# Kernel optimization log

Hardware: AMD Instinct MI355X
Metric: run time of the kernel (lower is better)

## Reference

```python
import jax, jax.numpy as jnp
import numpy as np

B, T = 128, 1024
V, H, L = 65, 512, 3


def setup_inputs() -> dict:
    key = jax.random.key(0)
    ks = jax.random.split(key, 8)
    s_in = 1.0 / np.sqrt(H)
    return {
        "x_seq": jax.random.randint(ks[0], (B, T), 0, V, dtype=jnp.int32),
        "emb": jax.random.normal(ks[1], (V, H), dtype=jnp.float32) * 0.02,
        "w_ih": jax.random.normal(ks[2], (L, 3 * H, H), dtype=jnp.float32) * s_in,
        "w_hh": jax.random.normal(ks[3], (L, 3 * H, H), dtype=jnp.float32) * s_in,
        "b": jax.random.normal(ks[4], (L, 3 * H), dtype=jnp.float32) * s_in,
        "b_n": jax.random.normal(ks[5], (L, H), dtype=jnp.float32) * s_in,
        "w_out": jax.random.normal(ks[6], (V, H), dtype=jnp.float32) * s_in,
        "b_out": jax.random.normal(ks[7], (V,), dtype=jnp.float32) * s_in,
    }


def _gru_cell(x, h, w_ih_l, w_hh_l, b_l, b_n_l):
    # eqx.nn.GRUCell math: igates = W_ih x + b ; hgates = W_hh h
    ig = x @ w_ih_l.T + b_l          # [B, 3H]
    hg = h @ w_hh_l.T                # [B, 3H]
    ir, iz, i_n = jnp.split(ig, 3, axis=-1)
    hr, hz, h_n = jnp.split(hg, 3, axis=-1)
    r = jax.nn.sigmoid(ir + hr)
    z = jax.nn.sigmoid(iz + hz)
    n = jnp.tanh(i_n + r * (h_n + b_n_l))
    return n + z * (h - n)


def reference(x_seq, emb, w_ih, w_hh, b, b_n, w_out, b_out):
    x_emb = emb[x_seq]                       # [B, T, H] embedding lookup
    x_tbh = jnp.swapaxes(x_emb, 0, 1)        # [T, B, H] scan over time
    h0 = jnp.zeros((L, x_seq.shape[0], H), dtype=x_emb.dtype)

    def step(hs, x):
        new_hs = []
        inp = x
        for i in range(L):                   # fixed small layer loop
            h = _gru_cell(inp, hs[i], w_ih[i], w_hh[i], b[i], b_n[i])
            new_hs.append(h)
            inp = h
        y = inp @ w_out.T + b_out            # [B, V]
        return jnp.stack(new_hs), y

    _, y_seq = jax.lax.scan(step, h0, x_tbh)  # y_seq: [T, B, V]
    return jnp.swapaxes(y_seq, 0, 1)          # [B, T, V]
```

## Files before the change

### kernel.cpp

```cpp
#include <hip/hip_runtime.h>

typedef _Float16 f16;
typedef _Float16 f16x8 __attribute__((ext_vector_type(8)));
typedef float f32x4 __attribute__((ext_vector_type(4)));

#define T_STEPS 1024
#define BATCH 128
#define HID 512
#define VOC 65
#define DRING 8
#define NLWG 192
#define NPWG 20
#define FPAD 16

#define OFF_READY 0
#define OFF_HRING 32768
#define HRING_BYTES (3*DRING*BATCH*HID*2)
#define OFF_WPACK (OFF_HRING + HRING_BYTES)
#define WPACK_BYTES (3*32*65536*2)
#define OFF_WOUT (OFF_WPACK + WPACK_BYTES)
#define WOUT_BYTES (5*16*512*2)
#define OFF_EMB (OFF_WOUT + WOUT_BYTES)

#define HHALF 32768

__device__ __forceinline__ float sigmoidf_(float x){ return 1.0f/(1.0f+__expf(-x)); }
__device__ __forceinline__ float tanhf_(float x){ return 1.0f - 2.0f/(__expf(2.0f*x)+1.0f); }

__device__ __forceinline__ f16x8 ld16_sc(const f16* p) {
  f16x8 r;
  asm volatile("global_load_dwordx4 %0, %1, off sc0 sc1" : "=v"(r) : "v"(p) : "memory");
  return r;
}
__device__ __forceinline__ f16x8 ld16_pl(const f16* p) {
  f16x8 r;
  asm volatile("global_load_dwordx4 %0, %1, off" : "=v"(r) : "v"(p) : "memory");
  return r;
}
__device__ __forceinline__ void st16_sc1(f16* p, f16x8 v){
  asm volatile("global_store_dwordx4 %0, %1, off sc1"::"v"(p),"v"(v):"memory"); }

__global__ void convert_kernel(const float* __restrict__ emb, const float* __restrict__ w_ih,
                               const float* __restrict__ w_hh, const float* __restrict__ w_out,
                               char* __restrict__ ws) {
  f16* wpack = (f16*)(ws + OFF_WPACK);
  f16* wout  = (f16*)(ws + OFF_WOUT);
  f16* embh  = (f16*)(ws + OFF_EMB);
  const int NW = 3*32*65536;
  const int TOT = NW + 40960 + VOC*HID;
  for (int e = blockIdx.x*blockDim.x + threadIdx.x; e < TOT; e += gridDim.x*blockDim.x) {
    if (e < NW) {
      int l = e >> 21, rem = e & 0x1FFFFF;
      int g = rem >> 16, idx = rem & 0xFFFF;
      int gt = idx >> 14, kc = (idx >> 9) & 31, lane = (idx >> 3) & 63, jj = idx & 7;
      int n = lane & 15, q = lane >> 4;
      int k = kc*32 + q*8 + jj, d = g*16 + n;
      int row = (gt==0) ? d : (gt==1) ? 512+d : 1024+d;
      float f = (k < 512) ? w_ih[((size_t)(l*1536+row)<<9) + k]
                          : w_hh[((size_t)(l*1536+row)<<9) + (k-512)];
      f16 h;
      if (gt < 3) h = (f16)f;
      else { f16 hi = (f16)f; h = (f16)((f - (float)hi)*2048.0f); }
      wpack[e] = h;
    } else if (e < NW + 40960) {
      int idx = e - NW;
      int vt = idx >> 13, r2 = idx & 8191;
      int kc = r2 >> 9, lane = (r2 >> 3) & 63, jj = r2 & 7;
      int n = lane & 15, q = lane >> 4;
      int v = vt*16 + n, k = kc*32 + q*8 + jj;
      wout[idx] = (v < VOC) ? (f16)w_out[((size_t)v<<9) + k] : (f16)0.0f;
    } else {
      int idx = e - NW - 40960;
      embh[idx] = (f16)emb[idx];
    }
  }
}

#define KEEP4(K0) asm volatile("" : "+v"(afr[K0]), "+v"(afr[K0+1]), "+v"(afr[K0+2]), "+v"(afr[K0+3]))

#define XCHUNK(K0, NW_) \
  asm volatile("s_waitcnt vmcnt(" #NW_ ")" ::: "memory"); \
  KEEP4(K0); \
  _Pragma("unroll") \
  for (int kc = K0; kc < K0+4; ++kc) { \
    f16x8 wnh = *(const f16x8*)(wlds + (((2*32 + kc)*64 + lane) << 3)); \
    f16x8 wnl = *(const f16x8*)(wlds + (((3*32 + kc)*64 + lane) << 3)); \
    ar   = __builtin_amdgcn_mfma_f32_16x16x32_f16(afr[kc], wr[kc], ar,   0, 0, 0); \
    az   = __builtin_amdgcn_mfma_f32_16x16x32_f16(afr[kc], wz[kc], az,   0, 0, 0); \
    anxh = __builtin_amdgcn_mfma_f32_16x16x32_f16(afr[kc], wnh,    anxh, 0, 0, 0); \
    anxl = __builtin_amdgcn_mfma_f32_16x16x32_f16(afr[kc], wnl,    anxl, 0, 0, 0); \
  }

#define HCHUNK(K0, NW_) \
  asm volatile("s_waitcnt vmcnt(" #NW_ ")" ::: "memory"); \
  KEEP4(K0); \
  _Pragma("unroll") \
  for (int kc = K0; kc < K0+4; ++kc) { \
    f16x8 wnh = *(const f16x8*)(wlds + (((2*32 + kc)*64 + lane) << 3)); \
    f16x8 wnl = *(const f16x8*)(wlds + (((3*32 + kc)*64 + lane) << 3)); \
    ar   = __builtin_amdgcn_mfma_f32_16x16x32_f16(afr[kc], wr[kc], ar,   0, 0, 0); \
    az   = __builtin_amdgcn_mfma_f32_16x16x32_f16(afr[kc], wz[kc], az,   0, 0, 0); \
    anhh = __builtin_amdgcn_mfma_f32_16x16x32_f16(afr[kc], wnh,    anhh, 0, 0, 0); \
    anhl = __builtin_amdgcn_mfma_f32_16x16x32_f16(afr[kc], wnl,    anhl, 0, 0, 0); \
  }

__global__ void __launch_bounds__(256) rnn_kernel(const int* __restrict__ xseq,
                           const float* __restrict__ bias, const float* __restrict__ bias_n,
                           const float* __restrict__ b_out, float* __restrict__ out,
                           char* __restrict__ ws) {
  int* F = (int*)(ws + OFF_READY);
  f16* hring = (f16*)(ws + OFF_HRING);
  const int wg = blockIdx.x;
  const int tid = threadIdx.x;
  const int lane = tid & 63, wv = tid >> 6;
  const int quad = lane >> 4, nlane = lane & 15;

  __shared__ __align__(16) f16 wlds[65536];
  __shared__ __align__(16) f16 wolds[8192];
  __shared__ __align__(16) f16 hstage[64*24];

  if (wg < NLWG) {
    const int l = wg / 64, r = wg % 64, g = r >> 1, bh = r & 1;
    {
      const f16x8* src = (const f16x8*)((const f16*)(ws + OFF_WPACK) + ((size_t)(l*32+g) << 16));
      f16x8* dst = (f16x8*)wlds;
      for (int i = tid; i < 8192; i += 256) dst[i] = src[i];
    }
    const int j = g*16 + nlane;
    const float br  = bias[l*1536 + j];
    const float bz  = bias[l*1536 + 512 + j];
    const float bin = bias[l*1536 + 1024 + j];
    const float bn  = bias_n[l*512 + j];
    const int bm = bh*64 + wv*16 + nlane;
    const int tofs = quad*512 + (wv*16 + nlane)*8;

    const int* selfp = F + (l*64 + bh*32 + (lane & 31))*FPAD;
    const int* upp   = (l > 0) ? (F + ((l-1)*64 + bh*32 + (lane & 31))*FPAD) : F;
    const int* bpp = F; int bpact = 0;
    if (wv == 1) {
      if (l < 2) { if (lane < 32) { bpp = F + ((l+1)*64 + bh*32 + lane)*FPAD; bpact = 1; } }
      else       { if (lane < 10) { bpp = F + (192 + bh*10 + lane)*FPAD;      bpact = 1; } }
    }
    __syncthreads();
    f16x8 wr[32], wz[32];
#pragma unroll
    for (int kc = 0; kc < 32; ++kc) {
      wr[kc] = *(const f16x8*)(wlds + (((0*32 + kc)*64 + lane) << 3));
      wz[kc] = *(const f16x8*)(wlds + (((1*32 + kc)*64 + lane) << 3));
    }
    const f16* embh = (const f16*)(ws + OFF_EMB);
    unsigned short hprev[4] = {0, 0, 0, 0};

    for (int t = 0; t < T_STEPS; ++t) {
      if (wv == 0) {
        if (l > 0 && lane >= 32) {
          const int tgt = t + 1;
          int spins = 0;
          while (1) {
            int v = __hip_atomic_load(upp, __ATOMIC_RELAXED, __HIP_MEMORY_SCOPE_AGENT);
            if (__all(v >= tgt)) break;
            if (++spins > (1 << 22)) break;
            __builtin_amdgcn_s_sleep(1);
          }
        }
      } else if (wv == 1) {
        const int tgt = t - (DRING-1);
        int spins = 0;
        while (1) {
          int v = 0x7FFFFFFF;
          if (bpact) v = __hip_atomic_load(bpp, __ATOMIC_RELAXED, __HIP_MEMORY_SCOPE_AGENT);
          if (__all(v >= tgt)) break;
          if (++spins > (1 << 22)) break;
          __builtin_amdgcn_s_sleep(1);
        }
      }
      __syncthreads();

      const int slot_w = t & (DRING-1), slot_r = (t + DRING - 1) & (DRING-1);
      f16x8 afr[32];
      if (l == 0) {
        int idx = xseq[bm*T_STEPS + t];
        const f16* xr = embh + (size_t)idx*HID + quad*8;
#pragma unroll
        for (int kc = 0; kc < 16; ++kc) afr[kc] = ld16_pl(xr + kc*32);
      } else {
        const f16* xr = hring + (size_t)(((l-1)*DRING + slot_w)*2 + bh)*HHALF + tofs;
#pragma unroll
        for (int kc = 0; kc < 16; ++kc) afr[kc] = ld16_sc(xr + kc*2048);
      }
      if (wv == 0 && lane < 32) {
        int spins = 0;
        while (1) {
          int v = __hip_atomic_load(selfp, __ATOMIC_RELAXED, __HIP_MEMORY_SCOPE_AGENT);
          if (__all(v >= t)) break;
          if (++spins > (1 << 22)) break;
          __builtin_amdgcn_s_sleep(1);
        }
      }
      __syncthreads();
      {
        const f16* hrk = hring + (size_t)((l*DRING + slot_r)*2 + bh)*HHALF + tofs;
#pragma unroll
        for (int kc = 0; kc < 16; ++kc) afr[16 + kc] = ld16_sc(hrk + kc*2048);
      }

      f32x4 ar{0,0,0,0}, az{0,0,0,0}, anxh{0,0,0,0}, anxl{0,0,0,0}, anhh{0,0,0,0}, anhl{0,0,0,0};
      XCHUNK(0, 28)  XCHUNK(4, 24)  XCHUNK(8, 20)   XCHUNK(12, 16)
      HCHUNK(16, 12) HCHUNK(20, 8)  HCHUNK(24, 4)   HCHUNK(28, 0)

#pragma unroll
      for (int i = 0; i < 4; ++i) {
        float rr = sigmoidf_(ar[i] + br);
        float zz = sigmoidf_(az[i] + bz);
        float hn = anhh[i] + anhl[i]*(1.0f/2048.0f) + bn;
        float nn = tanhf_(anxh[i] + anxl[i]*(1.0f/2048.0f) + bin + rr*hn);
        union { unsigned short u; f16 h; } cr; cr.u = hprev[i];
        float hv = nn + zz*((float)cr.h - nn);
        union { f16 h; unsigned short u; } cw; cw.h = (f16)hv;
        hprev[i] = cw.u;
        hstage[(wv*16 + quad*4 + i)*24 + nlane] = cw.h;
      }
      __syncthreads();
      if (tid < 128) {
        int d8i = tid >> 6, row = tid & 63;
        f16x8 v8 = *(const f16x8*)(hstage + row*24 + d8i*8);
        f16* hw = hring + (size_t)((l*DRING + slot_w)*2 + bh)*HHALF
                        + (size_t)(2*g + d8i)*512 + row*8;
        st16_sc1(hw, v8);
      }
      asm volatile("s_waitcnt vmcnt(0)" ::: "memory");
      __syncthreads();
      if (tid == 0)
        __hip_atomic_store(F + (l*64 + bh*32 + g)*FPAD, t + 1,
                           __ATOMIC_RELAXED, __HIP_MEMORY_SCOPE_AGENT);
    }
  } else if (wg < NLWG + NPWG) {
    const int p = wg - NLWG, bt = p / 5, vt = p % 5, half = bt >> 1;
    {
      const f16x8* src = (const f16x8*)((const f16*)(ws + OFF_WOUT) + vt*8192);
      f16x8* dst = (f16x8*)wolds;
      for (int i = tid; i < 1024; i += 256) dst[i] = src[i];
    }
    const int v = vt*16 + nlane;
    const float bo = (v < VOC) ? b_out[v] : 0.0f;
    __syncthreads();
    for (int t = 0; t < T_STEPS; ++t) {
      if (wv == 0) {
        const int tgt = t + 1;
        int spins = 0;
        while (1) {
          int vv = 0x7FFFFFFF;
          if (lane < 32) vv = __hip_atomic_load(F + (2*64 + half*32 + lane)*FPAD,
                                                __ATOMIC_RELAXED, __HIP_MEMORY_SCOPE_AGENT);
          if (__all(vv >= tgt)) break;
          if (++spins > (1 << 22)) break;
          __builtin_amdgcn_s_sleep(1);
        }
      }
      __syncthreads();
      if (wv < 2) {
        const int row_abs = bt*32 + wv*16 + nlane;
        const int bh2 = row_abs >> 6, rih = row_abs & 63;
        const f16* hrow = hring + (size_t)((2*DRING + (t & (DRING-1)))*2 + bh2)*HHALF
                                + quad*512 + rih*8;
        f16x8 af[16];
#pragma unroll
        for (int kc = 0; kc < 16; ++kc) af[kc] = ld16_sc(hrow + kc*2048);
        asm volatile("s_waitcnt vmcnt(0)" ::: "memory");
#pragma unroll
        for (int kc = 0; kc < 16; ++kc) asm volatile("" : "+v"(af[kc]));
        f32x4 acc{0,0,0,0};
#pragma unroll
        for (int kc = 0; kc < 16; ++kc) {
          f16x8 w = *(const f16x8*)(wolds + ((kc*64 + lane) << 3));
          acc = __builtin_amdgcn_mfma_f32_16x16x32_f16(af[kc], w, acc, 0, 0, 0);
        }
        if (v < VOC) {
          const int bmb = bt*32 + wv*16;
#pragma unroll
          for (int i = 0; i < 4; ++i) {
            int bidx = bmb + quad*4 + i;
            out[((size_t)bidx*T_STEPS + t)*VOC + v] = acc[i] + bo;
          }
        }
      }
      __syncthreads();
      if (tid == 0)
        __hip_atomic_store(F + (192 + p)*FPAD, t + 1, __ATOMIC_RELAXED, __HIP_MEMORY_SCOPE_AGENT);
    }
  }
}

extern "C" void kernel_launch(void* const* d_in, const int* in_sizes, int n_in,
                              void* d_out, int out_size, void* d_ws, size_t ws_size,
                              hipStream_t stream) {
  const int*   xseq  = (const int*)d_in[0];
  const float* emb   = (const float*)d_in[1];
  const float* w_ih  = (const float*)d_in[2];
  const float* w_hh  = (const float*)d_in[3];
  const float* b     = (const float*)d_in[4];
  const float* b_n   = (const float*)d_in[5];
  const float* w_out = (const float*)d_in[6];
  const float* b_out = (const float*)d_in[7];
  char* ws = (char*)d_ws;

  (void)hipMemsetAsync(d_ws, 0, OFF_HRING + HRING_BYTES, stream);
  hipLaunchKernelGGL(convert_kernel, dim3(4096), dim3(256), 0, stream,
                     emb, w_ih, w_hh, w_out, ws);
  hipLaunchKernelGGL(rnn_kernel, dim3(NLWG + NPWG), dim3(256), 0, stream,
                     xseq, b, b_n, b_out, (float*)d_out, ws);
}
```

Baseline: 6.919 ms.

## Map each layer/batch-half group onto one XCD and use acquire/release with plain loads

```diff
diff --git a/kernel.cpp b/kernel.cpp
--- a/kernel.cpp
+++ b/kernel.cpp
@@ -9,8 +9,6 @@
 #define HID 512
 #define VOC 65
 #define DRING 8
-#define NLWG 192
-#define NPWG 20
 #define FPAD 16
 
 #define OFF_READY 0
@@ -27,11 +25,6 @@
 __device__ __forceinline__ float sigmoidf_(float x){ return 1.0f/(1.0f+__expf(-x)); }
 __device__ __forceinline__ float tanhf_(float x){ return 1.0f - 2.0f/(__expf(2.0f*x)+1.0f); }
 
-__device__ __forceinline__ f16x8 ld16_sc(const f16* p) {
-  f16x8 r;
-  asm volatile("global_load_dwordx4 %0, %1, off sc0 sc1" : "=v"(r) : "v"(p) : "memory");
-  return r;
-}
 __device__ __forceinline__ f16x8 ld16_pl(const f16* p) {
   f16x8 r;
   asm volatile("global_load_dwordx4 %0, %1, off" : "=v"(r) : "v"(p) : "memory");
@@ -114,13 +107,14 @@
   const int tid = threadIdx.x;
   const int lane = tid & 63, wv = tid >> 6;
   const int quad = lane >> 4, nlane = lane & 15;
+  const int xcd = wg & 7, mem = wg >> 3;
 
   __shared__ __align__(16) f16 wlds[65536];
   __shared__ __align__(16) f16 wolds[8192];
   __shared__ __align__(16) f16 hstage[64*24];
 
-  if (wg < NLWG) {
-    const int l = wg / 64, r = wg % 64, g = r >> 1, bh = r & 1;
+  if (xcd < 6) {
+    const int gid = xcd, l = gid >> 1, bh = gid & 1, g = mem;
     {
       const f16x8* src = (const f16x8*)((const f16*)(ws + OFF_WPACK) + ((size_t)(l*32+g) << 16));
       f16x8* dst = (f16x8*)wlds;
@@ -135,7 +129,9 @@
     const int tofs = quad*512 + (wv*16 + nlane)*8;
 
     const int* selfp = F + (l*64 + bh*32 + (lane & 31))*FPAD;
+    const int* self0 = F + (l*64 + bh*32)*FPAD;
     const int* upp   = (l > 0) ? (F + ((l-1)*64 + bh*32 + (lane & 31))*FPAD) : F;
+    const int* up0   = (l > 0) ? (F + ((l-1)*64 + bh*32)*FPAD) : F;
     const int* bpp = F; int bpact = 0;
     if (wv == 1) {
       if (l < 2) { if (lane < 32) { bpp = F + ((l+1)*64 + bh*32 + lane)*FPAD; bpact = 1; } }
@@ -153,15 +149,18 @@
 
     for (int t = 0; t < T_STEPS; ++t) {
       if (wv == 0) {
-        if (l > 0 && lane >= 32) {
-          const int tgt = t + 1;
-          int spins = 0;
-          while (1) {
-            int v = __hip_atomic_load(upp, __ATOMIC_RELAXED, __HIP_MEMORY_SCOPE_AGENT);
-            if (__all(v >= tgt)) break;
-            if (++spins > (1 << 22)) break;
-            __builtin_amdgcn_s_sleep(1);
+        if (l > 0) {
+          if (lane >= 32) {
+            const int tgt = t + 1;
+            int spins = 0;
+            while (1) {
+              int v = __hip_atomic_load(upp, __ATOMIC_RELAXED, __HIP_MEMORY_SCOPE_AGENT);
+              if (__all(v >= tgt)) break;
+              if (++spins > (1 << 22)) break;
+              __builtin_amdgcn_s_sleep(1);
+            }
           }
+          (void)__hip_atomic_load(up0, __ATOMIC_ACQUIRE, __HIP_MEMORY_SCOPE_AGENT);
         }
       } else if (wv == 1) {
         const int tgt = t - (DRING-1);
@@ -186,22 +185,25 @@
       } else {
         const f16* xr = hring + (size_t)(((l-1)*DRING + slot_w)*2 + bh)*HHALF + tofs;
 #pragma unroll
-        for (int kc = 0; kc < 16; ++kc) afr[kc] = ld16_sc(xr + kc*2048);
-      }
-      if (wv == 0 && lane < 32) {
-        int spins = 0;
-        while (1) {
-          int v = __hip_atomic_load(selfp, __ATOMIC_RELAXED, __HIP_MEMORY_SCOPE_AGENT);
-          if (__all(v >= t)) break;
-          if (++spins > (1 << 22)) break;
-          __builtin_amdgcn_s_sleep(1);
-        }
+        for (int kc = 0; kc < 16; ++kc) afr[kc] = ld16_pl(xr + kc*2048);
+      }
+      if (wv == 0) {
+        if (lane < 32) {
+          int spins = 0;
+          while (1) {
+            int v = __hip_atomic_load(selfp, __ATOMIC_RELAXED, __HIP_MEMORY_SCOPE_AGENT);
+            if (__all(v >= t)) break;
+            if (++spins > (1 << 22)) break;
+            __builtin_amdgcn_s_sleep(1);
+          }
+        }
+        (void)__hip_atomic_load(self0, __ATOMIC_ACQUIRE, __HIP_MEMORY_SCOPE_AGENT);
       }
       __syncthreads();
       {
         const f16* hrk = hring + (size_t)((l*DRING + slot_r)*2 + bh)*HHALF + tofs;
 #pragma unroll
-        for (int kc = 0; kc < 16; ++kc) afr[16 + kc] = ld16_sc(hrk + kc*2048);
+        for (int kc = 0; kc < 16; ++kc) afr[16 + kc] = ld16_pl(hrk + kc*2048);
       }
 
       f32x4 ar{0,0,0,0}, az{0,0,0,0}, anxh{0,0,0,0}, anxl{0,0,0,0}, anhh{0,0,0,0}, anhl{0,0,0,0};
@@ -232,10 +234,10 @@
       __syncthreads();
       if (tid == 0)
         __hip_atomic_store(F + (l*64 + bh*32 + g)*FPAD, t + 1,
-                           __ATOMIC_RELAXED, __HIP_MEMORY_SCOPE_AGENT);
-    }
-  } else if (wg < NLWG + NPWG) {
-    const int p = wg - NLWG, bt = p / 5, vt = p % 5, half = bt >> 1;
+                           __ATOMIC_RELEASE, __HIP_MEMORY_SCOPE_AGENT);
+    }
+  } else if (xcd == 6 && mem < 20) {
+    const int p = mem, bt = p / 5, vt = p % 5, half = bt >> 1;
     {
       const f16x8* src = (const f16x8*)((const f16*)(ws + OFF_WOUT) + vt*8192);
       f16x8* dst = (f16x8*)wolds;
@@ -243,19 +245,22 @@
     }
     const int v = vt*16 + nlane;
     const float bo = (v < VOC) ? b_out[v] : 0.0f;
+    const int* l2p = F + (2*64 + half*32 + (lane & 31))*FPAD;
+    const int* l20 = F + (2*64 + half*32)*FPAD;
     __syncthreads();
     for (int t = 0; t < T_STEPS; ++t) {
       if (wv == 0) {
-        const int tgt = t + 1;
-        int spins = 0;
-        while (1) {
-          int vv = 0x7FFFFFFF;
-          if (lane < 32) vv = __hip_atomic_load(F + (2*64 + half*32 + lane)*FPAD,
-                                                __ATOMIC_RELAXED, __HIP_MEMORY_SCOPE_AGENT);
-          if (__all(vv >= tgt)) break;
-          if (++spins > (1 << 22)) break;
-          __builtin_amdgcn_s_sleep(1);
-        }
+        if (lane < 32) {
+          const int tgt = t + 1;
+          int spins = 0;
+          while (1) {
+            int vv = __hip_atomic_load(l2p, __ATOMIC_RELAXED, __HIP_MEMORY_SCOPE_AGENT);
+            if (__all(vv >= tgt)) break;
+            if (++spins > (1 << 22)) break;
+            __builtin_amdgcn_s_sleep(1);
+          }
+        }
+        (void)__hip_atomic_load(l20, __ATOMIC_ACQUIRE, __HIP_MEMORY_SCOPE_AGENT);
       }
       __syncthreads();
       if (wv < 2) {
@@ -265,7 +270,7 @@
                                 + quad*512 + rih*8;
         f16x8 af[16];
 #pragma unroll
-        for (int kc = 0; kc < 16; ++kc) af[kc] = ld16_sc(hrow + kc*2048);
+        for (int kc = 0; kc < 16; ++kc) af[kc] = ld16_pl(hrow + kc*2048);
         asm volatile("s_waitcnt vmcnt(0)" ::: "memory");
 #pragma unroll
         for (int kc = 0; kc < 16; ++kc) asm volatile("" : "+v"(af[kc]));
@@ -307,6 +312,6 @@
   (void)hipMemsetAsync(d_ws, 0, OFF_HRING + HRING_BYTES, stream);
   hipLaunchKernelGGL(convert_kernel, dim3(4096), dim3(256), 0, stream,
                      emb, w_ih, w_hh, w_out, ws);
-  hipLaunchKernelGGL(rnn_kernel, dim3(NLWG + NPWG), dim3(256), 0, stream,
+  hipLaunchKernelGGL(rnn_kernel, dim3(256), dim3(256), 0, stream,
                      xseq, b, b_n, b_out, (float*)d_out, ws);
 }
```

After: 10.74 ms. 1.55x slower.

## Map layer groups to XCDs and sync intra-XCD steps through L2

Applied to the files above, without the earlier changes.

```diff
diff --git a/kernel.cpp b/kernel.cpp
--- a/kernel.cpp
+++ b/kernel.cpp
@@ -9,11 +9,11 @@
 #define HID 512
 #define VOC 65
 #define DRING 8
-#define NLWG 192
-#define NPWG 20
 #define FPAD 16
 
 #define OFF_READY 0
+#define OFF_FL    16384
+#define OFF_CTL   28672
 #define OFF_HRING 32768
 #define HRING_BYTES (3*DRING*BATCH*HID*2)
 #define OFF_WPACK (OFF_HRING + HRING_BYTES)
@@ -32,13 +32,34 @@
   asm volatile("global_load_dwordx4 %0, %1, off sc0 sc1" : "=v"(r) : "v"(p) : "memory");
   return r;
 }
+__device__ __forceinline__ void st16_sc1(f16* p, f16x8 v){
+  asm volatile("global_store_dwordx4 %0, %1, off sc1"::"v"(p),"v"(v):"memory"); }
 __device__ __forceinline__ f16x8 ld16_pl(const f16* p) {
   f16x8 r;
   asm volatile("global_load_dwordx4 %0, %1, off" : "=v"(r) : "v"(p) : "memory");
   return r;
 }
-__device__ __forceinline__ void st16_sc1(f16* p, f16x8 v){
-  asm volatile("global_store_dwordx4 %0, %1, off sc1"::"v"(p),"v"(v):"memory"); }
+__device__ __forceinline__ void st16_pl(f16* p, f16x8 v){
+  asm volatile("global_store_dwordx4 %0, %1, off"::"v"(p),"v"(v):"memory"); }
+__device__ __forceinline__ f16x8 ld16_l2(const f16* p) {
+  f16x8 r;
+  asm volatile("global_load_dwordx4 %0, %1, off sc0" : "=v"(r) : "v"(p) : "memory");
+  return r;
+}
+__device__ __forceinline__ int ld4_sc(const int* p){
+  int r;
+  asm volatile("global_load_dword %0, %1, off sc0 sc1\n\ts_waitcnt vmcnt(0)" : "=v"(r) : "v"(p) : "memory");
+  return r;
+}
+__device__ __forceinline__ int ld4_l2(const int* p){
+  int r;
+  asm volatile("global_load_dword %0, %1, off sc0\n\ts_waitcnt vmcnt(0)" : "=v"(r) : "v"(p) : "memory");
+  return r;
+}
+__device__ __forceinline__ void st4_sc1(int* p, int v){
+  asm volatile("global_store_dword %0, %1, off sc1"::"v"(p),"v"(v):"memory"); }
+__device__ __forceinline__ void st4_pl(int* p, int v){
+  asm volatile("global_store_dword %0, %1, off"::"v"(p),"v"(v):"memory"); }
 
 __global__ void convert_kernel(const float* __restrict__ emb, const float* __restrict__ w_ih,
                                const float* __restrict__ w_hh, const float* __restrict__ w_out,
@@ -108,19 +129,22 @@
                            const float* __restrict__ bias, const float* __restrict__ bias_n,
                            const float* __restrict__ b_out, float* __restrict__ out,
                            char* __restrict__ ws) {
-  int* F = (int*)(ws + OFF_READY);
+  int* FC = (int*)(ws + OFF_READY);
+  int* FL = (int*)(ws + OFF_FL);
   f16* hring = (f16*)(ws + OFF_HRING);
   const int wg = blockIdx.x;
   const int tid = threadIdx.x;
   const int lane = tid & 63, wv = tid >> 6;
   const int quad = lane >> 4, nlane = lane & 15;
+  const int xcd = wg & 7, mem = wg >> 3;
 
   __shared__ __align__(16) f16 wlds[65536];
   __shared__ __align__(16) f16 wolds[8192];
   __shared__ __align__(16) f16 hstage[64*24];
-
-  if (wg < NLWG) {
-    const int l = wg / 64, r = wg % 64, g = r >> 1, bh = r & 1;
+  __shared__ int s_fast, s_bail;
+
+  if (xcd < 6) {
+    const int gid = xcd, l = gid >> 1, bh = gid & 1, g = mem;
     {
       const f16x8* src = (const f16x8*)((const f16*)(ws + OFF_WPACK) + ((size_t)(l*32+g) << 16));
       f16x8* dst = (f16x8*)wlds;
@@ -134,14 +158,77 @@
     const int bm = bh*64 + wv*16 + nlane;
     const int tofs = quad*512 + (wv*16 + nlane)*8;
 
-    const int* selfp = F + (l*64 + bh*32 + (lane & 31))*FPAD;
-    const int* upp   = (l > 0) ? (F + ((l-1)*64 + bh*32 + (lane & 31))*FPAD) : F;
-    const int* bpp = F; int bpact = 0;
+    const int fi = l*64 + bh*32;
+    const int* selfFCp = FC + (fi + (lane & 31))*FPAD;
+    const int* selfFLp = FL + (fi + (lane & 31))*FPAD;
+    const int* upp = (l > 0) ? (FC + ((l-1)*64 + bh*32 + (lane & 31))*FPAD) : FC;
+    const int* bpp = FC; int bpact = 0;
     if (wv == 1) {
-      if (l < 2) { if (lane < 32) { bpp = F + ((l+1)*64 + bh*32 + lane)*FPAD; bpact = 1; } }
-      else       { if (lane < 10) { bpp = F + (192 + bh*10 + lane)*FPAD;      bpact = 1; } }
+      if (l < 2) { if (lane < 32) { bpp = FC + ((l+1)*64 + bh*32 + lane)*FPAD; bpact = 1; } }
+      else       { if (lane < 10) { bpp = FC + (192 + bh*10 + lane)*FPAD;      bpact = 1; } }
+    }
+
+    if (tid == 0) {
+      int* TS = (int*)(ws + OFF_CTL) + gid*64;
+      int* VT = (int*)(ws + OFF_CTL) + 6*64 + gid*32;
+      int* MD = (int*)(ws + OFF_CTL) + 6*64 + 6*32;
+      int ok = 1;
+      st4_pl(TS + g, 100 + g);
+      {
+        int spins = 0;
+        while (1) {
+          int good = 1;
+          for (int m = 0; m < 32; ++m) {
+            int v = ld4_l2(TS + m);
+            if (v != 100 + m && v != 200 + m) { good = 0; break; }
+          }
+          if (good) break;
+          if (++spins > (1 << 10)) { ok = 0; break; }
+          __builtin_amdgcn_s_sleep(2);
+        }
+      }
+      if (ok) {
+        st4_pl(TS + g, 200 + g);
+        int spins = 0;
+        while (1) {
+          int good = 1;
+          for (int m = 0; m < 32; ++m) { if (ld4_l2(TS + m) != 200 + m) { good = 0; break; } }
+          if (good) break;
+          if (++spins > (1 << 10)) { ok = 0; break; }
+          __builtin_amdgcn_s_sleep(2);
+        }
+      }
+      st4_sc1((int*)VT + g, 1 + ok);
+      int fast = 0;
+      if (g == 0) {
+        int spins = 0, allf;
+        while (1) {
+          int seen = 1; allf = 1;
+          for (int m = 0; m < 32; ++m) {
+            int v = ld4_sc(VT + m);
+            if (v == 0) { seen = 0; break; }
+            if (v != 2) allf = 0;
+          }
+          if (seen) break;
+          if (++spins > (1 << 9)) { allf = 0; break; }
+          __builtin_amdgcn_s_sleep(4);
+        }
+        fast = allf;
+        st4_sc1(MD + gid, 1 + fast);
+      } else {
+        int spins = 0;
+        while (1) {
+          int v = ld4_sc(MD + gid);
+          if (v != 0) { fast = (v == 2); break; }
+          if (++spins > (1 << 16)) { fast = 0; break; }
+          __builtin_amdgcn_s_sleep(8);
+        }
+      }
+      s_fast = fast; s_bail = 0;
     }
     __syncthreads();
+    const int fast = s_fast;
+
     f16x8 wr[32], wz[32];
 #pragma unroll
     for (int kc = 0; kc < 32; ++kc) {
@@ -155,22 +242,24 @@
       if (wv == 0) {
         if (l > 0 && lane >= 32) {
           const int tgt = t + 1;
+          const int cap = s_bail ? (1<<8) : (1<<22);
           int spins = 0;
           while (1) {
             int v = __hip_atomic_load(upp, __ATOMIC_RELAXED, __HIP_MEMORY_SCOPE_AGENT);
             if (__all(v >= tgt)) break;
-            if (++spins > (1 << 22)) break;
+            if (++spins > cap) { s_bail = 1; break; }
             __builtin_amdgcn_s_sleep(1);
           }
         }
       } else if (wv == 1) {
         const int tgt = t - (DRING-1);
+        const int cap = s_bail ? (1<<8) : (1<<22);
         int spins = 0;
         while (1) {
           int v = 0x7FFFFFFF;
           if (bpact) v = __hip_atomic_load(bpp, __ATOMIC_RELAXED, __HIP_MEMORY_SCOPE_AGENT);
           if (__all(v >= tgt)) break;
-          if (++spins > (1 << 22)) break;
+          if (++spins > cap) { s_bail = 1; break; }
           __builtin_amdgcn_s_sleep(1);
         }
       }
@@ -189,19 +278,36 @@
         for (int kc = 0; kc < 16; ++kc) afr[kc] = ld16_sc(xr + kc*2048);
       }
       if (wv == 0 && lane < 32) {
-        int spins = 0;
-        while (1) {
-          int v = __hip_atomic_load(selfp, __ATOMIC_RELAXED, __HIP_MEMORY_SCOPE_AGENT);
-          if (__all(v >= t)) break;
-          if (++spins > (1 << 22)) break;
-          __builtin_amdgcn_s_sleep(1);
+        if (fast) {
+          const int cap = s_bail ? (1<<8) : (1<<18);
+          int spins = 0;
+          while (1) {
+            int v = ld4_l2(selfFLp);
+            if (__all(v >= t)) break;
+            if (++spins > cap) { s_bail = 1; break; }
+            __builtin_amdgcn_s_sleep(1);
+          }
+        } else {
+          const int cap = s_bail ? (1<<8) : (1<<22);
+          int spins = 0;
+          while (1) {
+            int v = __hip_atomic_load(selfFCp, __ATOMIC_RELAXED, __HIP_MEMORY_SCOPE_AGENT);
+            if (__all(v >= t)) break;
+            if (++spins > cap) { s_bail = 1; break; }
+            __builtin_amdgcn_s_sleep(1);
+          }
         }
       }
       __syncthreads();
       {
         const f16* hrk = hring + (size_t)((l*DRING + slot_r)*2 + bh)*HHALF + tofs;
-#pragma unroll
-        for (int kc = 0; kc < 16; ++kc) afr[16 + kc] = ld16_sc(hrk + kc*2048);
+        if (fast) {
+#pragma unroll
+          for (int kc = 0; kc < 16; ++kc) afr[16 + kc] = ld16_l2(hrk + kc*2048);
+        } else {
+#pragma unroll
+          for (int kc = 0; kc < 16; ++kc) afr[16 + kc] = ld16_sc(hrk + kc*2048);
+        }
       }
 
       f32x4 ar{0,0,0,0}, az{0,0,0,0}, anxh{0,0,0,0}, anxl{0,0,0,0}, anhh{0,0,0,0}, anhl{0,0,0,0};
@@ -221,21 +327,28 @@
         hstage[(wv*16 + quad*4 + i)*24 + nlane] = cw.h;
       }
       __syncthreads();
-      if (tid < 128) {
-        int d8i = tid >> 6, row = tid & 63;
+      if (tid >= 128) {
+        int ts2 = tid - 128, d8i = ts2 >> 6, row = ts2 & 63;
         f16x8 v8 = *(const f16x8*)(hstage + row*24 + d8i*8);
         f16* hw = hring + (size_t)((l*DRING + slot_w)*2 + bh)*HHALF
                         + (size_t)(2*g + d8i)*512 + row*8;
-        st16_sc1(hw, v8);
-      }
-      asm volatile("s_waitcnt vmcnt(0)" ::: "memory");
-      __syncthreads();
-      if (tid == 0)
-        __hip_atomic_store(F + (l*64 + bh*32 + g)*FPAD, t + 1,
-                           __ATOMIC_RELAXED, __HIP_MEMORY_SCOPE_AGENT);
-    }
-  } else if (wg < NLWG + NPWG) {
-    const int p = wg - NLWG, bt = p / 5, vt = p % 5, half = bt >> 1;
+        if (fast) { st16_pl(hw, v8); st16_sc1(hw, v8);
+                    asm volatile("s_waitcnt vmcnt(1)" ::: "memory"); }
+        else      { st16_sc1(hw, v8);
+                    asm volatile("s_waitcnt vmcnt(0)" ::: "memory"); }
+      }
+      __syncthreads();
+      if (tid == 128) {
+        if (fast) { st4_pl (FL + (fi + g)*FPAD, t + 1);
+                    st4_sc1(FC + (fi + g)*FPAD, t); }
+        else      { st4_sc1(FC + (fi + g)*FPAD, t + 1); }
+      }
+    }
+    if (tid >= 128) asm volatile("s_waitcnt vmcnt(0)" ::: "memory");
+    __syncthreads();
+    if (tid == 128) st4_sc1(FC + (fi + g)*FPAD, T_STEPS);
+  } else if (xcd == 6 && mem < 20) {
+    const int p = mem, bt = p / 5, vt = p % 5, half = bt >> 1;
     {
       const f16x8* src = (const f16x8*)((const f16*)(ws + OFF_WOUT) + vt*8192);
       f16x8* dst = (f16x8*)wolds;
@@ -243,17 +356,19 @@
     }
     const int v = vt*16 + nlane;
     const float bo = (v < VOC) ? b_out[v] : 0.0f;
+    if (tid == 0) s_bail = 0;
     __syncthreads();
     for (int t = 0; t < T_STEPS; ++t) {
       if (wv == 0) {
         const int tgt = t + 1;
+        const int cap = s_bail ? (1<<8) : (1<<22);
         int spins = 0;
         while (1) {
           int vv = 0x7FFFFFFF;
-          if (lane < 32) vv = __hip_atomic_load(F + (2*64 + half*32 + lane)*FPAD,
+          if (lane < 32) vv = __hip_atomic_load((int*)(ws + OFF_READY) + (2*64 + half*32 + lane)*FPAD,
                                                 __ATOMIC_RELAXED, __HIP_MEMORY_SCOPE_AGENT);
           if (__all(vv >= tgt)) break;
-          if (++spins > (1 << 22)) break;
+          if (++spins > cap) { s_bail = 1; break; }
           __builtin_amdgcn_s_sleep(1);
         }
       }
@@ -286,7 +401,7 @@
       }
       __syncthreads();
       if (tid == 0)
-        __hip_atomic_store(F + (192 + p)*FPAD, t + 1, __ATOMIC_RELAXED, __HIP_MEMORY_SCOPE_AGENT);
+        st4_sc1((int*)(ws + OFF_READY) + (192 + p)*FPAD, t + 1);
     }
   }
 }
@@ -307,6 +422,6 @@
   (void)hipMemsetAsync(d_ws, 0, OFF_HRING + HRING_BYTES, stream);
   hipLaunchKernelGGL(convert_kernel, dim3(4096), dim3(256), 0, stream,
                      emb, w_ih, w_hh, w_out, ws);
-  hipLaunchKernelGGL(rnn_kernel, dim3(NLWG + NPWG), dim3(256), 0, stream,
+  hipLaunchKernelGGL(rnn_kernel, dim3(256), dim3(256), 0, stream,
                      xseq, b, b_n, b_out, (float*)d_out, ws);
 }
```

Measured after the change: 10.10 ms. 46.0% more time.
